# Optimization experiments

Measured on AMD Instinct MI355X. Metric: run time of the kernel, lower is better.

The kernel has to match this reference:

```python
import jax, jax.numpy as jnp
import numpy as np

B, D, G, H = 65536, 512, 16, 128


def setup_inputs() -> dict:
    key = jax.random.key(0)
    ks = jax.random.split(key, 8)
    s = 1.0 / np.sqrt(D)
    sh = 1.0 / np.sqrt(H)
    return {
        "z": jax.random.normal(ks[0], (B, D), dtype=jnp.float32),
        "Wc": jax.random.uniform(ks[1], (D, G), jnp.float32, -s, s),
        "bc": jax.random.uniform(ks[2], (G,), jnp.float32, -s, s),
        "W1": jax.random.uniform(ks[3], (G, D, H), jnp.float32, -s, s),
        "b1": jax.random.uniform(ks[4], (G, H), jnp.float32, -s, s),
        "W2": jax.random.uniform(ks[5], (G, H), jnp.float32, -sh, sh),
        "b2": jax.random.uniform(ks[6], (G,), jnp.float32, -sh, sh),
    }


def reference(z, Wc, bc, W1, b1, W2, b2):
    # classifier head + softmax
    logits = z @ Wc + bc                                  # [B, G]
    p_g = jax.nn.softmax(logits, axis=1)                  # [B, G]
    # G experts fused as one batched GEMM: fc1 -> GELU -> fc2 (dropout = identity at eval)
    h = jax.nn.gelu(jnp.einsum('bd,gdh->bgh', z, W1) + b1, approximate=False)  # [B, G, H]
    y_all = jnp.einsum('bgh,gh->bg', h, W2) + b2          # [B, G]
    return logits, p_g, y_all
```

## Files before the change

### kernel.cpp

```cpp
#include <hip/hip_runtime.h>
#include <cstdint>
#include <cstddef>

typedef __bf16 bf16x8 __attribute__((ext_vector_type(8)));
typedef float f32x4 __attribute__((ext_vector_type(4)));
typedef unsigned short ushortx8 __attribute__((ext_vector_type(8)));

__device__ __forceinline__ unsigned short f2bf(float f) {
  union { float f; unsigned int u; } v; v.f = f;
  return (unsigned short)((v.u + 0x8000u) >> 16);
}

__device__ __forceinline__ float gelu_f(float x) {
  float t = 0.7978845608f * x * (1.0f + 0.044715f * x * x);
  float e = __expf(-2.0f * fabsf(t));
  float th = (1.0f - e) / (1.0f + e);
  th = (t >= 0.0f) ? th : -th;
  return 0.5f * x * (1.0f + th);
}

#define GLOAD16(gsrc, ldst)                                                  \
  __builtin_amdgcn_global_load_lds(                                          \
      (const __attribute__((address_space(1))) unsigned int*)(gsrc),         \
      (__attribute__((address_space(3))) unsigned int*)(uintptr_t)(          \
          (char*)(ldst)),                                                    \
      16, 0, 0)

#define SWZ_FRAG(base, R, C8)                                                \
  (*(const bf16x8*)((base) + (((R) >> 5) * 4096) +                           \
                    ((((R)&31) * 8 + ((C8) ^ ((R)&7))) * 16)))

__global__ __launch_bounds__(256) void k_convert(
    const float* __restrict__ z, const float* __restrict__ W1,
    const float* __restrict__ Wc, unsigned short* __restrict__ zb,
    unsigned short* __restrict__ w1t, unsigned short* __restrict__ wct) {
  int bid = blockIdx.x;
  int tid = threadIdx.x;
  if (bid < 16384) {
    size_t i = ((size_t)bid * 256 + tid) * 8;
    const float4* p = (const float4*)(z + i);
    float4 a = p[0], b = p[1];
    ushortx8 r;
    r[0] = f2bf(a.x); r[1] = f2bf(a.y); r[2] = f2bf(a.z); r[3] = f2bf(a.w);
    r[4] = f2bf(b.x); r[5] = f2bf(b.y); r[6] = f2bf(b.z); r[7] = f2bf(b.w);
    *(ushortx8*)(zb + i) = r;
  } else if (bid < 16384 + 1024) {
    __shared__ float tile[32][33];
    int b = bid - 16384;
    int gg = b >> 6;
    int t = b & 63;
    int d0 = (t >> 2) * 32;
    int h0 = (t & 3) * 32;
    int tx = tid & 31, ty = tid >> 5;
#pragma unroll
    for (int r = 0; r < 4; ++r) {
      int d = d0 + r * 8 + ty;
      tile[r * 8 + ty][tx] = W1[(gg << 16) + d * 128 + h0 + tx];
    }
    __syncthreads();
#pragma unroll
    for (int r = 0; r < 4; ++r) {
      int h = h0 + r * 8 + ty;
      w1t[(gg << 16) + h * 512 + d0 + tx] = f2bf(tile[tx][r * 8 + ty]);
    }
  } else {
#pragma unroll
    for (int j = 0; j < 32; ++j) {
      int i = j * 256 + tid;
      wct[(i & 15) * 512 + (i >> 4)] = f2bf(Wc[i]);
    }
  }
}

__global__ __launch_bounds__(256, 2) void k_main(
    const unsigned short* __restrict__ zb,
    const unsigned short* __restrict__ w1t,
    const unsigned short* __restrict__ wct,
    const float* __restrict__ bc, const float* __restrict__ b1,
    const float* __restrict__ w2, const float* __restrict__ b2,
    float* __restrict__ out) {
  __shared__ alignas(16) char lds[16384 + 32768];
  const int tid = threadIdx.x;
  const int p = blockIdx.x >> 9;
  const int m = blockIdx.x & 511;
  const int mbase = m * 128;
  const int wv = tid >> 6;
  const int ln = tid & 63;
  const int l15 = ln & 15;
  const int l4 = ln >> 4;

  const int c8s = (((tid & 7) ^ ((tid >> 3) & 7))) * 8;
  const unsigned short* ag = zb + (size_t)(mbase + (tid >> 3)) * 512 + c8s;
  char* ldsB = lds + 16384;

  if (p < 8) {
    const unsigned short* bg =
        w1t + p * 131072 + (tid >> 3) * 512 + c8s;
    const int wr = wv >> 1;
    const int wc = wv & 1;
    const int e = p * 2 + wc;
    const int rowb = wr * 64;
    const int colb = wc * 128;
    f32x4 acc[4][8] = {};
    for (int kt = 0; kt < 8; ++kt) {
      const int ko = kt * 64;
#pragma unroll
      for (int it = 0; it < 4; ++it)
        GLOAD16(ag + (size_t)it * 32 * 512 + ko, lds + it * 4096 + tid * 16);
#pragma unroll
      for (int it = 0; it < 8; ++it)
        GLOAD16(bg + it * 32 * 512 + ko, ldsB + it * 4096 + tid * 16);
      __syncthreads();
#pragma unroll
      for (int ks = 0; ks < 2; ++ks) {
        bf16x8 af[4];
#pragma unroll
        for (int rt = 0; rt < 4; ++rt)
          af[rt] = SWZ_FRAG(lds, rowb + rt * 16 + l15, ks * 4 + l4);
#pragma unroll
        for (int ct = 0; ct < 8; ++ct) {
          bf16x8 bf = SWZ_FRAG(ldsB, colb + ct * 16 + l15, ks * 4 + l4);
#pragma unroll
          for (int rt = 0; rt < 4; ++rt)
            acc[rt][ct] = __builtin_amdgcn_mfma_f32_16x16x32_bf16(
                af[rt], bf, acc[rt][ct], 0, 0, 0);
        }
      }
      __syncthreads();
    }
    float b1v[8], w2v[8];
#pragma unroll
    for (int ct = 0; ct < 8; ++ct) {
      int n = ct * 16 + l15;
      b1v[ct] = b1[e * 128 + n];
      w2v[ct] = w2[e * 128 + n];
    }
    float b2v = b2[e];
#pragma unroll
    for (int rt = 0; rt < 4; ++rt) {
#pragma unroll
      for (int i = 0; i < 4; ++i) {
        float s = 0.0f;
#pragma unroll
        for (int ct = 0; ct < 8; ++ct) {
          float x = acc[rt][ct][i] + b1v[ct];
          s += gelu_f(x) * w2v[ct];
        }
#pragma unroll
        for (int off = 1; off < 16; off <<= 1)
          s += __shfl_xor(s, off, 16);
        if (l15 == 0) {
          int row = rowb + rt * 16 + l4 * 4 + i;
          out[(size_t)2097152 + (size_t)(mbase + row) * 16 + e] = s + b2v;
        }
      }
    }
  } else {
#pragma unroll
    for (int it = 0; it < 4; ++it)
      GLOAD16(wct + it * 2048 + tid * 8, ldsB + it * 4096 + tid * 16);
    f32x4 acc2[2] = {};
    for (int kt = 0; kt < 8; ++kt) {
      const int ko = kt * 64;
#pragma unroll
      for (int it = 0; it < 4; ++it)
        GLOAD16(ag + (size_t)it * 32 * 512 + ko, lds + it * 4096 + tid * 16);
      __syncthreads();
      bf16x8 bfr[2];
#pragma unroll
      for (int ks = 0; ks < 2; ++ks)
        bfr[ks] = *(const bf16x8*)(ldsB + l15 * 1024 +
                                   (ko + ks * 32 + l4 * 8) * 2);
#pragma unroll
      for (int rt = 0; rt < 2; ++rt)
#pragma unroll
        for (int ks = 0; ks < 2; ++ks) {
          bf16x8 af = SWZ_FRAG(lds, wv * 32 + rt * 16 + l15, ks * 4 + l4);
          acc2[rt] = __builtin_amdgcn_mfma_f32_16x16x32_bf16(af, bfr[ks],
                                                             acc2[rt], 0, 0, 0);
        }
      __syncthreads();
    }
    float bcv = bc[l15];
#pragma unroll
    for (int rt = 0; rt < 2; ++rt) {
#pragma unroll
      for (int i = 0; i < 4; ++i) {
        int row = wv * 32 + rt * 16 + l4 * 4 + i;
        float lg = acc2[rt][i] + bcv;
        float mx = lg;
#pragma unroll
        for (int off = 1; off < 16; off <<= 1)
          mx = fmaxf(mx, __shfl_xor(mx, off, 16));
        float ex = __expf(lg - mx);
        float sm = ex;
#pragma unroll
        for (int off = 1; off < 16; off <<= 1)
          sm += __shfl_xor(sm, off, 16);
        size_t ro = (size_t)(mbase + row) * 16 + l15;
        out[ro] = lg;
        out[1048576 + ro] = ex / sm;
      }
    }
  }
}

extern "C" void kernel_launch(void* const* d_in, const int* in_sizes, int n_in,
                              void* d_out, int out_size, void* d_ws,
                              size_t ws_size, hipStream_t stream) {
  const float* z = (const float*)d_in[0];
  const float* Wc = (const float*)d_in[1];
  const float* bc = (const float*)d_in[2];
  const float* W1 = (const float*)d_in[3];
  const float* b1 = (const float*)d_in[4];
  const float* W2 = (const float*)d_in[5];
  const float* b2 = (const float*)d_in[6];
  float* out = (float*)d_out;

  unsigned short* zb = (unsigned short*)d_ws;
  unsigned short* w1t = zb + (size_t)65536 * 512;
  unsigned short* wct = w1t + (size_t)16 * 128 * 512;

  k_convert<<<16384 + 1024 + 1, 256, 0, stream>>>(z, W1, Wc, zb, w1t, wct);
  k_main<<<9 * 512, 256, 0, stream>>>(zb, w1t, wct, bc, b1, W2, b2, out);
}
```

Before: 429.6 us.

## Load expert weight fragments directly from global into registers, reorder block mapping

Weight (B operand) tiles for the expert GEMM and the classifier are no longer staged through LDS. Each lane now reads its MFMA fragment straight from global/L2 into registers, which cuts LDS from 48KB to 16KB and removes LDS writes for B. Block indexing is changed so the 9 blocks that share one z tile run next to each other, which should improve L2 reuse of z. The cost is many uncoalesced 16-byte global loads per lane and higher register pressure from holding 16 B fragments.

```diff
diff --git a/kernel.cpp b/kernel.cpp
--- a/kernel.cpp
+++ b/kernel.cpp
@@ -79,10 +79,10 @@
     const float* __restrict__ bc, const float* __restrict__ b1,
     const float* __restrict__ w2, const float* __restrict__ b2,
     float* __restrict__ out) {
-  __shared__ alignas(16) char lds[16384 + 32768];
+  __shared__ alignas(16) char lds[16384];
   const int tid = threadIdx.x;
-  const int p = blockIdx.x >> 9;
-  const int m = blockIdx.x & 511;
+  const int m = blockIdx.x / 9;
+  const int p = blockIdx.x % 9;
   const int mbase = m * 128;
   const int wv = tid >> 6;
   const int ln = tid & 63;
@@ -91,41 +91,57 @@
 
   const int c8s = (((tid & 7) ^ ((tid >> 3) & 7))) * 8;
   const unsigned short* ag = zb + (size_t)(mbase + (tid >> 3)) * 512 + c8s;
-  char* ldsB = lds + 16384;
 
   if (p < 8) {
-    const unsigned short* bg =
-        w1t + p * 131072 + (tid >> 3) * 512 + c8s;
     const int wr = wv >> 1;
     const int wc = wv & 1;
     const int e = p * 2 + wc;
     const int rowb = wr * 64;
-    const int colb = wc * 128;
+    const unsigned short* bb[8];
+#pragma unroll
+    for (int ct = 0; ct < 8; ++ct)
+      bb[ct] = w1t + e * 65536 + (ct * 16 + l15) * 512 + l4 * 8;
+    const int ab0 =
+        (rowb >> 5) * 4096 + (l15 * 8 + (l4 ^ (l15 & 7))) * 16;
+    const int ab1 =
+        (rowb >> 5) * 4096 + (l15 * 8 + ((4 + l4) ^ (l15 & 7))) * 16;
+
     f32x4 acc[4][8] = {};
     for (int kt = 0; kt < 8; ++kt) {
       const int ko = kt * 64;
 #pragma unroll
       for (int it = 0; it < 4; ++it)
-        GLOAD16(ag + (size_t)it * 32 * 512 + ko, lds + it * 4096 + tid * 16);
-#pragma unroll
-      for (int it = 0; it < 8; ++it)
-        GLOAD16(bg + it * 32 * 512 + ko, ldsB + it * 4096 + tid * 16);
-      __syncthreads();
-#pragma unroll
-      for (int ks = 0; ks < 2; ++ks) {
-        bf16x8 af[4];
+        GLOAD16(ag + it * 32 * 512 + ko, lds + it * 4096 + tid * 16);
+      bf16x8 bf0[8];
+#pragma unroll
+      for (int ct = 0; ct < 8; ++ct)
+        bf0[ct] = *(const bf16x8*)(bb[ct] + ko);
+      __syncthreads();
+      bf16x8 af[4];
+#pragma unroll
+      for (int rt = 0; rt < 4; ++rt)
+        af[rt] = *(const bf16x8*)(lds + ab0 + (rt >> 1) * 4096 +
+                                  (rt & 1) * 2048);
+      bf16x8 bf1[8];
+#pragma unroll
+      for (int ct = 0; ct < 8; ++ct)
+        bf1[ct] = *(const bf16x8*)(bb[ct] + ko + 32);
+#pragma unroll
+      for (int ct = 0; ct < 8; ++ct)
 #pragma unroll
         for (int rt = 0; rt < 4; ++rt)
-          af[rt] = SWZ_FRAG(lds, rowb + rt * 16 + l15, ks * 4 + l4);
-#pragma unroll
-        for (int ct = 0; ct < 8; ++ct) {
-          bf16x8 bf = SWZ_FRAG(ldsB, colb + ct * 16 + l15, ks * 4 + l4);
-#pragma unroll
-          for (int rt = 0; rt < 4; ++rt)
-            acc[rt][ct] = __builtin_amdgcn_mfma_f32_16x16x32_bf16(
-                af[rt], bf, acc[rt][ct], 0, 0, 0);
-        }
-      }
+          acc[rt][ct] = __builtin_amdgcn_mfma_f32_16x16x32_bf16(
+              af[rt], bf0[ct], acc[rt][ct], 0, 0, 0);
+#pragma unroll
+      for (int rt = 0; rt < 4; ++rt)
+        af[rt] = *(const bf16x8*)(lds + ab1 + (rt >> 1) * 4096 +
+                                  (rt & 1) * 2048);
+#pragma unroll
+      for (int ct = 0; ct < 8; ++ct)
+#pragma unroll
+        for (int rt = 0; rt < 4; ++rt)
+          acc[rt][ct] = __builtin_amdgcn_mfma_f32_16x16x32_bf16(
+              af[rt], bf1[ct], acc[rt][ct], 0, 0, 0);
       __syncthreads();
     }
     float b1v[8], w2v[8];
@@ -156,29 +172,25 @@
       }
     }
   } else {
-#pragma unroll
-    for (int it = 0; it < 4; ++it)
-      GLOAD16(wct + it * 2048 + tid * 8, ldsB + it * 4096 + tid * 16);
+    const unsigned short* wb = wct + l15 * 512 + l4 * 8;
     f32x4 acc2[2] = {};
     for (int kt = 0; kt < 8; ++kt) {
       const int ko = kt * 64;
 #pragma unroll
       for (int it = 0; it < 4; ++it)
-        GLOAD16(ag + (size_t)it * 32 * 512 + ko, lds + it * 4096 + tid * 16);
-      __syncthreads();
-      bf16x8 bfr[2];
-#pragma unroll
-      for (int ks = 0; ks < 2; ++ks)
-        bfr[ks] = *(const bf16x8*)(ldsB + l15 * 1024 +
-                                   (ko + ks * 32 + l4 * 8) * 2);
-#pragma unroll
-      for (int rt = 0; rt < 2; ++rt)
-#pragma unroll
-        for (int ks = 0; ks < 2; ++ks) {
-          bf16x8 af = SWZ_FRAG(lds, wv * 32 + rt * 16 + l15, ks * 4 + l4);
-          acc2[rt] = __builtin_amdgcn_mfma_f32_16x16x32_bf16(af, bfr[ks],
-                                                             acc2[rt], 0, 0, 0);
-        }
+        GLOAD16(ag + it * 32 * 512 + ko, lds + it * 4096 + tid * 16);
+      bf16x8 bfr0 = *(const bf16x8*)(wb + ko);
+      bf16x8 bfr1 = *(const bf16x8*)(wb + ko + 32);
+      __syncthreads();
+#pragma unroll
+      for (int rt = 0; rt < 2; ++rt) {
+        bf16x8 a0 = SWZ_FRAG(lds, wv * 32 + rt * 16 + l15, l4);
+        acc2[rt] = __builtin_amdgcn_mfma_f32_16x16x32_bf16(a0, bfr0, acc2[rt],
+                                                           0, 0, 0);
+        bf16x8 a1 = SWZ_FRAG(lds, wv * 32 + rt * 16 + l15, 4 + l4);
+        acc2[rt] = __builtin_amdgcn_mfma_f32_16x16x32_bf16(a1, bfr1, acc2[rt],
+                                                           0, 0, 0);
+      }
       __syncthreads();
     }
     float bcv = bc[l15];
@@ -222,5 +234,5 @@
   unsigned short* wct = w1t + (size_t)16 * 128 * 512;
 
   k_convert<<<16384 + 1024 + 1, 256, 0, stream>>>(z, W1, Wc, zb, w1t, wct);
-  k_main<<<9 * 512, 256, 0, stream>>>(zb, w1t, wct, bc, b1, W2, b2, out);
-}
+  k_main<<<512 * 9, 256, 0, stream>>>(zb, w1t, wct, bc, b1, W2, b2, out);
+}
```

After: 535.2 us. 1.25x slower.

## Shrink expert GEMM tile to 64 rows, cheaper GELU, more occupancy

Applied to the files above, without the earlier changes.

The expert GEMM block tile drops from 128 to 64 rows. Each wave now covers one expert half of 64 columns, and the two halves are combined through a small LDS buffer before the y_all store. This cuts the accumulator registers enough to raise launch bounds to 3 blocks per SM. The tanh-based GELU is replaced by a sigmoid-form approximation built on exp2 and rcp intrinsics, trimming VALU work. The classifier path now loads Wc fragments straight from global memory instead of staging them in LDS, and the classifier blocks are placed first in the grid. In exchange, the z tile is reloaded twice as often across blocks.

```diff
diff --git a/kernel.cpp b/kernel.cpp
--- a/kernel.cpp
+++ b/kernel.cpp
@@ -11,12 +11,11 @@
   return (unsigned short)((v.u + 0x8000u) >> 16);
 }
 
-__device__ __forceinline__ float gelu_f(float x) {
-  float t = 0.7978845608f * x * (1.0f + 0.044715f * x * x);
-  float e = __expf(-2.0f * fabsf(t));
-  float th = (1.0f - e) / (1.0f + e);
-  th = (t >= 0.0f) ? th : -th;
-  return 0.5f * x * (1.0f + th);
+__device__ __forceinline__ float gelu_s(float x) {
+  float x2 = x * x;
+  float p = __builtin_fmaf(x2, -0.10294324f, -2.30220819f);
+  float e = __builtin_amdgcn_exp2f(x * p);
+  return x * __builtin_amdgcn_rcpf(1.0f + e);
 }
 
 #define GLOAD16(gsrc, ldst)                                                  \
@@ -72,41 +71,36 @@
   }
 }
 
-__global__ __launch_bounds__(256, 2) void k_main(
+__global__ __launch_bounds__(256, 3) void k_main(
     const unsigned short* __restrict__ zb,
     const unsigned short* __restrict__ w1t,
     const unsigned short* __restrict__ wct,
     const float* __restrict__ bc, const float* __restrict__ b1,
     const float* __restrict__ w2, const float* __restrict__ b2,
     float* __restrict__ out) {
-  __shared__ alignas(16) char lds[16384 + 32768];
+  __shared__ alignas(16) char lds[8192 + 32768 + 1024];
   const int tid = threadIdx.x;
-  const int p = blockIdx.x >> 9;
-  const int m = blockIdx.x & 511;
-  const int mbase = m * 128;
-  const int wv = tid >> 6;
+  const int wq = tid >> 6;
   const int ln = tid & 63;
   const int l15 = ln & 15;
   const int l4 = ln >> 4;
-
   const int c8s = (((tid & 7) ^ ((tid >> 3) & 7))) * 8;
-  const unsigned short* ag = zb + (size_t)(mbase + (tid >> 3)) * 512 + c8s;
-  char* ldsB = lds + 16384;
-
-  if (p < 8) {
-    const unsigned short* bg =
-        w1t + p * 131072 + (tid >> 3) * 512 + c8s;
-    const int wr = wv >> 1;
-    const int wc = wv & 1;
-    const int e = p * 2 + wc;
-    const int rowb = wr * 64;
-    const int colb = wc * 128;
-    f32x4 acc[4][8] = {};
+  char* ldsB = lds + 8192;
+
+  if (blockIdx.x >= 512) {
+    const int eb = blockIdx.x - 512;
+    const int p = eb >> 10;
+    const int mbase = (eb & 1023) * 64;
+    const unsigned short* ag = zb + (size_t)(mbase + (tid >> 3)) * 512 + c8s;
+    const unsigned short* bg = w1t + p * 131072 + (tid >> 3) * 512 + c8s;
+    const int e = p * 2 + (wq >> 1);
+    const int nb = (wq & 1) * 64;
+    f32x4 acc[4][4] = {};
     for (int kt = 0; kt < 8; ++kt) {
       const int ko = kt * 64;
 #pragma unroll
-      for (int it = 0; it < 4; ++it)
-        GLOAD16(ag + (size_t)it * 32 * 512 + ko, lds + it * 4096 + tid * 16);
+      for (int it = 0; it < 2; ++it)
+        GLOAD16(ag + it * 32 * 512 + ko, lds + it * 4096 + tid * 16);
 #pragma unroll
       for (int it = 0; it < 8; ++it)
         GLOAD16(bg + it * 32 * 512 + ko, ldsB + it * 4096 + tid * 16);
@@ -116,10 +110,10 @@
         bf16x8 af[4];
 #pragma unroll
         for (int rt = 0; rt < 4; ++rt)
-          af[rt] = SWZ_FRAG(lds, rowb + rt * 16 + l15, ks * 4 + l4);
-#pragma unroll
-        for (int ct = 0; ct < 8; ++ct) {
-          bf16x8 bf = SWZ_FRAG(ldsB, colb + ct * 16 + l15, ks * 4 + l4);
+          af[rt] = SWZ_FRAG(lds, rt * 16 + l15, ks * 4 + l4);
+#pragma unroll
+        for (int ct = 0; ct < 4; ++ct) {
+          bf16x8 bf = SWZ_FRAG(ldsB, wq * 64 + ct * 16 + l15, ks * 4 + l4);
 #pragma unroll
           for (int rt = 0; rt < 4; ++rt)
             acc[rt][ct] = __builtin_amdgcn_mfma_f32_16x16x32_bf16(
@@ -128,57 +122,57 @@
       }
       __syncthreads();
     }
-    float b1v[8], w2v[8];
-#pragma unroll
-    for (int ct = 0; ct < 8; ++ct) {
-      int n = ct * 16 + l15;
+    float b1v[4], w2v[4];
+#pragma unroll
+    for (int ct = 0; ct < 4; ++ct) {
+      int n = nb + ct * 16 + l15;
       b1v[ct] = b1[e * 128 + n];
       w2v[ct] = w2[e * 128 + n];
     }
-    float b2v = b2[e];
+    float* ylds = (float*)(lds + 40960);
 #pragma unroll
     for (int rt = 0; rt < 4; ++rt) {
 #pragma unroll
       for (int i = 0; i < 4; ++i) {
         float s = 0.0f;
 #pragma unroll
-        for (int ct = 0; ct < 8; ++ct) {
-          float x = acc[rt][ct][i] + b1v[ct];
-          s += gelu_f(x) * w2v[ct];
-        }
+        for (int ct = 0; ct < 4; ++ct)
+          s += gelu_s(acc[rt][ct][i] + b1v[ct]) * w2v[ct];
 #pragma unroll
         for (int off = 1; off < 16; off <<= 1)
           s += __shfl_xor(s, off, 16);
-        if (l15 == 0) {
-          int row = rowb + rt * 16 + l4 * 4 + i;
-          out[(size_t)2097152 + (size_t)(mbase + row) * 16 + e] = s + b2v;
-        }
-      }
+        if (l15 == 0) ylds[wq * 64 + rt * 16 + l4 * 4 + i] = s;
+      }
+    }
+    __syncthreads();
+    if (tid < 128) {
+      int row = tid & 63, ee = tid >> 6;
+      float y = ylds[ee * 128 + row] + ylds[ee * 128 + 64 + row] +
+                b2[p * 2 + ee];
+      out[(size_t)2097152 + (size_t)(mbase + row) * 16 + p * 2 + ee] = y;
     }
   } else {
-#pragma unroll
-    for (int it = 0; it < 4; ++it)
-      GLOAD16(wct + it * 2048 + tid * 8, ldsB + it * 4096 + tid * 16);
+    const int mbase = blockIdx.x * 128;
+    const unsigned short* ag = zb + (size_t)(mbase + (tid >> 3)) * 512 + c8s;
+    const unsigned short* wb = wct + l15 * 512 + l4 * 8;
     f32x4 acc2[2] = {};
     for (int kt = 0; kt < 8; ++kt) {
       const int ko = kt * 64;
 #pragma unroll
       for (int it = 0; it < 4; ++it)
-        GLOAD16(ag + (size_t)it * 32 * 512 + ko, lds + it * 4096 + tid * 16);
-      __syncthreads();
-      bf16x8 bfr[2];
-#pragma unroll
-      for (int ks = 0; ks < 2; ++ks)
-        bfr[ks] = *(const bf16x8*)(ldsB + l15 * 1024 +
-                                   (ko + ks * 32 + l4 * 8) * 2);
-#pragma unroll
-      for (int rt = 0; rt < 2; ++rt)
-#pragma unroll
-        for (int ks = 0; ks < 2; ++ks) {
-          bf16x8 af = SWZ_FRAG(lds, wv * 32 + rt * 16 + l15, ks * 4 + l4);
-          acc2[rt] = __builtin_amdgcn_mfma_f32_16x16x32_bf16(af, bfr[ks],
-                                                             acc2[rt], 0, 0, 0);
-        }
+        GLOAD16(ag + it * 32 * 512 + ko, lds + it * 4096 + tid * 16);
+      bf16x8 bfr0 = *(const bf16x8*)(wb + ko);
+      bf16x8 bfr1 = *(const bf16x8*)(wb + ko + 32);
+      __syncthreads();
+#pragma unroll
+      for (int rt = 0; rt < 2; ++rt) {
+        bf16x8 a0 = SWZ_FRAG(lds, wq * 32 + rt * 16 + l15, l4);
+        acc2[rt] = __builtin_amdgcn_mfma_f32_16x16x32_bf16(a0, bfr0, acc2[rt],
+                                                           0, 0, 0);
+        bf16x8 a1 = SWZ_FRAG(lds, wq * 32 + rt * 16 + l15, 4 + l4);
+        acc2[rt] = __builtin_amdgcn_mfma_f32_16x16x32_bf16(a1, bfr1, acc2[rt],
+                                                           0, 0, 0);
+      }
       __syncthreads();
     }
     float bcv = bc[l15];
@@ -186,7 +180,7 @@
     for (int rt = 0; rt < 2; ++rt) {
 #pragma unroll
       for (int i = 0; i < 4; ++i) {
-        int row = wv * 32 + rt * 16 + l4 * 4 + i;
+        int row = wq * 32 + rt * 16 + l4 * 4 + i;
         float lg = acc2[rt][i] + bcv;
         float mx = lg;
 #pragma unroll
@@ -222,5 +216,6 @@
   unsigned short* wct = w1t + (size_t)16 * 128 * 512;
 
   k_convert<<<16384 + 1024 + 1, 256, 0, stream>>>(z, W1, Wc, zb, w1t, wct);
-  k_main<<<9 * 512, 256, 0, stream>>>(zb, w1t, wct, bc, b1, W2, b2, out);
-}
+  k_main<<<512 + 8 * 1024, 256, 0, stream>>>(zb, w1t, wct, bc, b1, W2, b2,
+                                             out);
+}
```

Result: faster. 401.4 us (-6.6%).
